# Optimization experiments

Measured on AMD Instinct MI355X. Metric: run time of the kernel, lower is better.

## Reference

```python
import jax, jax.numpy as jnp
import numpy as np

N, E, D, C, H1 = 100000, 1600000, 64, 8, 2


def setup_inputs() -> dict:
    key = jax.random.key(0)
    ks = jax.random.split(key, 16)
    s = 0.1  # small init scale
    inp = {}
    inp["x"] = jax.random.normal(ks[0], (N, D), jnp.float32)
    inp["edge_index"] = jax.random.randint(ks[1], (2, E), 0, N, dtype=jnp.int64)
    # conv1: GATConv(D, D, heads=2, concat=True)
    inp["W1"] = jax.random.normal(ks[2], (D, H1 * D), jnp.float32) * s
    inp["a_src1"] = jax.random.normal(ks[3], (H1, D), jnp.float32) * s
    inp["a_dst1"] = jax.random.normal(ks[4], (H1, D), jnp.float32) * s
    inp["b1"] = jnp.zeros((H1 * D,), jnp.float32)
    # conv2: GATConv(2D, D, heads=1, concat=False)
    inp["W2"] = jax.random.normal(ks[5], (H1 * D, D), jnp.float32) * s
    inp["a_src2"] = jax.random.normal(ks[6], (1, D), jnp.float32) * s
    inp["a_dst2"] = jax.random.normal(ks[7], (1, D), jnp.float32) * s
    inp["b2"] = jnp.zeros((D,), jnp.float32)
    # mlp head (Z = D since G=0)
    inp["mlp1_w"] = jax.random.normal(ks[8], (D, D), jnp.float32) * s
    inp["mlp1_b"] = jnp.zeros((D,), jnp.float32)
    inp["mlp2_w"] = jax.random.normal(ks[9], (D, C), jnp.float32) * s
    inp["mlp2_b"] = jnp.zeros((C,), jnp.float32)
    return inp


def _segment_softmax(e, dst, n):
    # numerically-stable softmax over edges grouped by destination node
    m = jax.ops.segment_max(e, dst, num_segments=n)
    ex = jnp.exp(e - m[dst])
    z = jax.ops.segment_sum(ex, dst, num_segments=n)
    return ex / (z[dst] + 1e-16)


def _gat_conv(x, ei, W, a_src, a_dst, b, heads, f_out, concat):
    n = x.shape[0]
    h = (x @ W).reshape(n, heads, f_out)            # [N,H,F]
    alpha_s = jnp.einsum('nhf,hf->nh', h, a_src)     # [N,H]
    alpha_d = jnp.einsum('nhf,hf->nh', h, a_dst)
    src, dst = ei[0], ei[1]
    e = jax.nn.leaky_relu(alpha_s[src] + alpha_d[dst], 0.2)  # [E,H]
    alpha = _segment_softmax(e, dst, n)
    out = jax.ops.segment_sum(h[src] * alpha[:, :, None], dst, num_segments=n)
    out = out.reshape(n, heads * f_out) if concat else out.mean(axis=1)
    return out + b


def reference(x, edge_index, W1, a_src1, a_dst1, b1, W2, a_src2, a_dst2, b2,
              mlp1_w, mlp1_b, mlp2_w, mlp2_b):
    n = x.shape[0]
    loops = jnp.arange(n, dtype=edge_index.dtype)
    ei = jnp.concatenate([edge_index, jnp.stack([loops, loops])], axis=1)
    h = jax.nn.elu(_gat_conv(x, ei, W1, a_src1, a_dst1, b1, H1, D, True))
    h = jax.nn.elu(_gat_conv(h, ei, W2, a_src2, a_dst2, b2, 1, D, False))
    h = jax.nn.relu(h @ mlp1_w + mlp1_b)
    return jax.nn.relu(h @ mlp2_w + mlp2_b)
```

## Files before the change

kernel.cpp:

```cpp
#include <hip/hip_runtime.h>
#include <hip/hip_bf16.h>

#define NN 100000
#define EE 1600000
#define MM 1700000
#define CH 8192
#define NBLK 208
#define N1 106496
#define NBKT 391
#define NCONV 38024

typedef unsigned short u16;
typedef __attribute__((ext_vector_type(8))) short bf16x8;
typedef __attribute__((ext_vector_type(4))) float f32x4;
typedef __attribute__((ext_vector_type(2))) float f32x2v;

__device__ __forceinline__ float bf2f(u16 u){ return __uint_as_float(((unsigned)u) << 16); }
__device__ __forceinline__ float bf2f_lo(unsigned u){ return __uint_as_float(u << 16); }
__device__ __forceinline__ float bf2f_hi(unsigned u){ return __uint_as_float(u & 0xFFFF0000u); }

__device__ __forceinline__ unsigned f2bf(float f){
  unsigned x = __float_as_uint(f);
  unsigned r = x + 0x7FFFu + ((x >> 16) & 1u);
  return (r >> 16);
}

__device__ __forceinline__ float wred(float v){
  v += __shfl_xor(v, 32, 64);
  v += __shfl_xor(v, 16, 64);
  v += __shfl_xor(v, 8, 64);
  v += __shfl_xor(v, 4, 64);
  v += __shfl_xor(v, 2, 64);
  v += __shfl_xor(v, 1, 64);
  return v;
}

__device__ __forceinline__ float eluf(float v){ return (v > 0.f) ? v : (__expf(v) - 1.f); }

__device__ __forceinline__ void acc_bf8p(f32x2v* acc, uint4 q, float w){
  f32x2v wv = {w, w};
  f32x2v h0 = {bf2f_lo(q.x), bf2f_hi(q.x)};
  f32x2v h1 = {bf2f_lo(q.y), bf2f_hi(q.y)};
  f32x2v h2 = {bf2f_lo(q.z), bf2f_hi(q.z)};
  f32x2v h3 = {bf2f_lo(q.w), bf2f_hi(q.w)};
  acc[0] += wv * h0;
  acc[1] += wv * h1;
  acc[2] += wv * h2;
  acc[3] += wv * h3;
}

__global__ void k_detect(const u16* __restrict__ x16, const int* __restrict__ ei32,
                         int* __restrict__ flags){
  int t = threadIdx.x;
  u16 u = x16[2 * t];
  int eb = (u >> 8) & 0x7F;
  int m1 = (eb >= 0x3A && eb <= 0x41) ? 1 : 0;
  int m2 = (ei32[2 * t + 1] == 0) ? 1 : 0;
  unsigned long long b1 = __ballot(m1);
  unsigned long long b2 = __ballot(m2);
  __shared__ int c1[2], c2[2];
  if ((t & 63) == 0){ c1[t >> 6] = __popcll(b1); c2[t >> 6] = __popcll(b2); }
  __syncthreads();
  if (t == 0){
    flags[0] = (c1[0] + c1[1] >= 64) ? 1 : 0;
    flags[1] = (c2[0] + c2[1] >= 64) ? 1 : 0;
  }
}

__global__ void k_fill(float* __restrict__ o, int n){
  int i = blockIdx.x * blockDim.x + threadIdx.x;
  if (i < n) o[i] = 12345.0f;
}

__global__ __launch_bounds__(256) void k_hist1(const int* __restrict__ ei, int* __restrict__ ghist,
                        const void* s0, const void* s1, const void* s2, const void* s3,
                        const void* s4, const void* s5, const void* s6, const void* s7,
                        const void* s8, const void* s9, const void* s10, const void* s11,
                        float* __restrict__ dst, u16* __restrict__ wt1, u16* __restrict__ wt2,
                        const int* __restrict__ flags){
  __shared__ int h[512];
  int b = blockIdx.x;
  if (b < NBLK){
    for (int i = threadIdx.x; i < 512; i += 256) h[i] = 0;
    __syncthreads();
    int base = b * CH;
    int i64 = flags[1];
    #pragma unroll 4
    for (int k = 0; k < CH / 256; ++k){
      int i = base + k * 256 + threadIdx.x;
      if (i < MM){
        int d;
        if (i < EE) d = i64 ? ei[2 * (EE + i)] : ei[EE + i];
        else        d = i - EE;
        atomicAdd(&h[d >> 8], 1);
      }
    }
    __syncthreads();
    for (int i = threadIdx.x; i < 512; i += 256) ghist[i * NBLK + b] = h[i];
    return;
  }
  int i = (b - NBLK) * 256 + threadIdx.x;
  if (i >= NCONV) return;
  int bf = flags[0];
  if (i < 21640){
    const int offs[13] = {0,8192,8320,8448,8576,16768,16832,16896,16960,21056,21120,21632,21640};
    const void* srcs[12] = {s0,s1,s2,s3,s4,s5,s6,s7,s8,s9,s10,s11};
    int seg = 0;
    while (i >= offs[seg + 1]) seg++;
    int j = i - offs[seg];
    float v = bf ? bf2f(((const u16*)srcs[seg])[j]) : ((const float*)srcs[seg])[j];
    dst[i] = v;
  } else if (i < 29832){
    int i2 = i - 21640;
    int c = i2 >> 6, k = i2 & 63;
    int si = k * 128 + c;
    wt1[i2] = bf ? ((const u16*)s0)[si] : (u16)f2bf(((const float*)s0)[si]);
  } else {
    int i3 = i - 29832;
    int c = i3 >> 7, k = i3 & 127;
    int si = k * 64 + c;
    wt2[i3] = bf ? ((const u16*)s4)[si] : (u16)f2bf(((const float*)s4)[si]);
  }
}

__global__ __launch_bounds__(1024) void k_gscan1(const int* __restrict__ ghist, int* __restrict__ incl,
                                                 int* __restrict__ bsums){
  __shared__ int s[1024];
  int i = blockIdx.x * 1024 + threadIdx.x;
  int v = (i < N1) ? ghist[i] : 0;
  s[threadIdx.x] = v;
  __syncthreads();
  for (int off = 1; off < 1024; off <<= 1){
    int t = (threadIdx.x >= off) ? s[threadIdx.x - off] : 0;
    __syncthreads();
    s[threadIdx.x] += t;
    __syncthreads();
  }
  if (i < N1) incl[i] = s[threadIdx.x];
  if (threadIdx.x == 1023) bsums[blockIdx.x] = s[1023];
}

__global__ void k_scan2(int* __restrict__ bsums, int nb){
  __shared__ int s[128];
  int t = threadIdx.x;
  int v = (t < nb) ? bsums[t] : 0;
  s[t] = v;
  __syncthreads();
  for (int off = 1; off < 128; off <<= 1){
    int x = (t >= off) ? s[t - off] : 0;
    __syncthreads();
    s[t] += x;
    __syncthreads();
  }
  if (t < nb) bsums[t] = s[t];
}

__global__ __launch_bounds__(256) void k_gscan3(const int* __restrict__ incl, const int* __restrict__ ghist,
                                                const int* __restrict__ bsums, int* __restrict__ off1){
  int i = blockIdx.x * blockDim.x + threadIdx.x;
  if (i >= N1) return;
  int b = i >> 10;
  int base = b ? bsums[b - 1] : 0;
  off1[i] = base + incl[i] - ghist[i];
}

__global__ __launch_bounds__(256) void k_scatter1(const int* __restrict__ ei, const int* __restrict__ off1,
                                                  unsigned* __restrict__ e1, const int* __restrict__ flags){
  __shared__ int offs[512];
  __shared__ int cnt[512];
  int b = blockIdx.x;
  for (int i = threadIdx.x; i < 512; i += 256){
    offs[i] = off1[i * NBLK + b];
    cnt[i] = 0;
  }
  __syncthreads();
  int base = b * CH;
  int i64 = flags[1];
  #pragma unroll 4
  for (int k = 0; k < CH / 256; ++k){
    int i = base + k * 256 + threadIdx.x;
    if (i >= MM) break;
    int d, s;
    if (i < EE){
      if (i64){ d = ei[2 * (EE + i)]; s = ei[2 * i]; }
      else    { d = ei[EE + i];       s = ei[i]; }
    } else { d = i - EE; s = d; }
    int bin = d >> 8;
    int r = atomicAdd(&cnt[bin], 1);
    e1[offs[bin] + r] = ((unsigned)s << 8) | ((unsigned)d & 255u);
  }
}

__global__ __launch_bounds__(256) void k_pass2(const unsigned* __restrict__ e1, const int* __restrict__ off1,
                                               int* __restrict__ csr, int* __restrict__ rp){
  __shared__ int hh[256];
  __shared__ int cc[256];
  int bu = blockIdx.x;
  int t = threadIdx.x;
  int s = off1[bu * NBLK];
  int e = off1[(bu + 1) * NBLK];
  hh[t] = 0; cc[t] = 0;
  __syncthreads();
  for (int j = s + t; j < e; j += 256)
    atomicAdd(&hh[e1[j] & 255u], 1);
  __syncthreads();
  int own = hh[t];
  for (int off = 1; off < 256; off <<= 1){
    int x = (t >= off) ? hh[t - off] : 0;
    __syncthreads();
    hh[t] += x;
    __syncthreads();
  }
  int excl = hh[t] - own;
  hh[t] = excl;
  int node = (bu << 8) + t;
  if (node < NN) rp[node] = s + excl;
  if (bu == 0 && t == 0) rp[NN] = MM;
  __syncthreads();
  for (int j = s + t; j < e; j += 256){
    unsigned kv = e1[j];
    int d = kv & 255u;
    int r = atomicAdd(&cc[d], 1);
    csr[s + hh[d] + r] = (int)(kv >> 8);
  }
}

__global__ __launch_bounds__(256) void k_gemm1(const void* __restrict__ xv, const u16* __restrict__ wt1,
                                               const float* __restrict__ asw, const float* __restrict__ adw,
                                               u16* __restrict__ h1bf, float* __restrict__ AS, float* __restrict__ AD,
                                               const int* __restrict__ flags, int n){
  int tid = threadIdx.x;
  int wv = tid >> 6, l = tid & 63;
  int lm = l & 15, lk = l >> 4;
  int M0 = blockIdx.x * 64 + wv * 16;
  int row = M0 + lm; if (row >= n) row = n - 1;
  bf16x8 a0, a1;
  if (flags[0]){
    const u16* xp = (const u16*)xv + (size_t)row * 64;
    union { uint4 u; bf16x8 v; } c0, c1;
    c0.u = *(const uint4*)&xp[lk * 8];
    c1.u = *(const uint4*)&xp[32 + lk * 8];
    a0 = c0.v; a1 = c1.v;
  } else {
    const float* xp = (const float*)xv + (size_t)row * 64;
    float4 f0 = *(const float4*)&xp[lk * 8];
    float4 f1 = *(const float4*)&xp[lk * 8 + 4];
    float4 f2 = *(const float4*)&xp[32 + lk * 8];
    float4 f3 = *(const float4*)&xp[32 + lk * 8 + 4];
    union { u16 s[8]; bf16x8 v; } p0, p1;
    p0.s[0]=(u16)f2bf(f0.x); p0.s[1]=(u16)f2bf(f0.y); p0.s[2]=(u16)f2bf(f0.z); p0.s[3]=(u16)f2bf(f0.w);
    p0.s[4]=(u16)f2bf(f1.x); p0.s[5]=(u16)f2bf(f1.y); p0.s[6]=(u16)f2bf(f1.z); p0.s[7]=(u16)f2bf(f1.w);
    p1.s[0]=(u16)f2bf(f2.x); p1.s[1]=(u16)f2bf(f2.y); p1.s[2]=(u16)f2bf(f2.z); p1.s[3]=(u16)f2bf(f2.w);
    p1.s[4]=(u16)f2bf(f3.x); p1.s[5]=(u16)f2bf(f3.y); p1.s[6]=(u16)f2bf(f3.z); p1.s[7]=(u16)f2bf(f3.w);
    a0 = p0.v; a1 = p1.v;
  }
  f32x4 acc[8];
  #pragma unroll
  for (int nt = 0; nt < 8; ++nt) acc[nt] = (f32x4){0.f, 0.f, 0.f, 0.f};
  #pragma unroll
  for (int nt = 0; nt < 8; ++nt){
    int col = nt * 16 + lm;
    union { uint4 u; bf16x8 v; } b0, b1;
    b0.u = *(const uint4*)&wt1[(size_t)col * 64 + lk * 8];
    b1.u = *(const uint4*)&wt1[(size_t)col * 64 + 32 + lk * 8];
    acc[nt] = __builtin_amdgcn_mfma_f32_16x16x32_bf16(a0, b0.v, acc[nt], 0, 0, 0);
    acc[nt] = __builtin_amdgcn_mfma_f32_16x16x32_bf16(a1, b1.v, acc[nt], 0, 0, 0);
  }
  float ps0[4] = {0,0,0,0}, pd0[4] = {0,0,0,0}, ps1[4] = {0,0,0,0}, pd1[4] = {0,0,0,0};
  #pragma unroll
  for (int nt = 0; nt < 8; ++nt){
    int col = nt * 16 + lm;
    float aw = asw[col], dw = adw[col];
    #pragma unroll
    for (int i = 0; i < 4; ++i){
      float v = acc[nt][i];
      if (nt < 4){ ps0[i] += v * aw; pd0[i] += v * dw; }
      else       { ps1[i] += v * aw; pd1[i] += v * dw; }
    }
  }
  #pragma unroll
  for (int mk = 8; mk >= 1; mk >>= 1){
    #pragma unroll
    for (int i = 0; i < 4; ++i){
      ps0[i] += __shfl_xor(ps0[i], mk, 64); pd0[i] += __shfl_xor(pd0[i], mk, 64);
      ps1[i] += __shfl_xor(ps1[i], mk, 64); pd1[i] += __shfl_xor(pd1[i], mk, 64);
    }
  }
  #pragma unroll
  for (int nt = 0; nt < 8; ++nt){
    int col = nt * 16 + lm;
    #pragma unroll
    for (int i = 0; i < 4; ++i){
      int r = M0 + lk * 4 + i;
      if (r < n) h1bf[(size_t)r * 128 + col] = (u16)f2bf(acc[nt][i]);
    }
  }
  if (lm == 0){
    #pragma unroll
    for (int i = 0; i < 4; ++i){
      int r = M0 + lk * 4 + i;
      if (r < n){
        AS[r * 2] = ps0[i]; AS[r * 2 + 1] = ps1[i];
        AD[r * 2] = pd0[i]; AD[r * 2 + 1] = pd1[i];
      }
    }
  }
}

__global__ __launch_bounds__(256) void k_agg1(const u16* __restrict__ h1bf, const int* __restrict__ rp,
                                              const int* __restrict__ csr, const float* __restrict__ AS,
                                              const float* __restrict__ AD, const float* __restrict__ b1,
                                              u16* __restrict__ out, int n){
  int node = (blockIdx.x * blockDim.x + threadIdx.x) >> 6;
  int lane = threadIdx.x & 63;
  if (node >= n) return;
  int g = lane >> 4, u = lane & 15;
  int beg = rp[node], end = rp[node + 1];
  float2 adv = *(const float2*)&AD[node * 2];
  f32x2v acc[4] = {{0,0},{0,0},{0,0},{0,0}};
  float zp0 = 0.f, zp1 = 0.f;
  for (int c = beg; c < end; c += 64){
    int m = end - c; if (m > 64) m = 64;
    int s_l = 0; float w0_l = 0.f, w1_l = 0.f;
    if (lane < m){
      s_l = csr[c + lane];
      float2 as2 = *(const float2*)&AS[s_l * 2];
      float e0 = as2.x + adv.x; e0 = fmaxf(e0, 0.2f * e0);
      float e1 = as2.y + adv.y; e1 = fmaxf(e1, 0.2f * e1);
      w0_l = __expf(e0); w1_l = __expf(e1);
    }
    zp0 += w0_l; zp1 += w1_l;
    for (int jj = 0; jj < m; jj += 16){
      int eA = jj + g, eB = jj + 4 + g, eC = jj + 8 + g, eD = jj + 12 + g;
      bool vA = eA < m, vB = eB < m, vC = eC < m, vD = eD < m;
      int sA = __shfl(s_l, eA, 64), sB = __shfl(s_l, eB, 64);
      int sC = __shfl(s_l, eC, 64), sD = __shfl(s_l, eD, 64);
      float wA0 = __shfl(w0_l, eA, 64), wA1 = __shfl(w1_l, eA, 64);
      float wB0 = __shfl(w0_l, eB, 64), wB1 = __shfl(w1_l, eB, 64);
      float wC0 = __shfl(w0_l, eC, 64), wC1 = __shfl(w1_l, eC, 64);
      float wD0 = __shfl(w0_l, eD, 64), wD1 = __shfl(w1_l, eD, 64);
      uint4 qA, qB, qC, qD;
      if (vA) qA = *(const uint4*)&h1bf[(size_t)sA * 128 + u * 8];
      if (vB) qB = *(const uint4*)&h1bf[(size_t)sB * 128 + u * 8];
      if (vC) qC = *(const uint4*)&h1bf[(size_t)sC * 128 + u * 8];
      if (vD) qD = *(const uint4*)&h1bf[(size_t)sD * 128 + u * 8];
      if (vA) acc_bf8p(acc, qA, (u < 8) ? wA0 : wA1);
      if (vB) acc_bf8p(acc, qB, (u < 8) ? wB0 : wB1);
      if (vC) acc_bf8p(acc, qC, (u < 8) ? wC0 : wC1);
      if (vD) acc_bf8p(acc, qD, (u < 8) ? wD0 : wD1);
    }
  }
  #pragma unroll
  for (int mk = 16; mk <= 32; mk <<= 1){
    #pragma unroll
    for (int k = 0; k < 4; ++k){
      acc[k][0] += __shfl_xor(acc[k][0], mk, 64);
      acc[k][1] += __shfl_xor(acc[k][1], mk, 64);
    }
  }
  float z0 = wred(zp0), z1 = wred(zp1);
  float rz = (u < 8) ? (1.f / (z0 + 1e-16f)) : (1.f / (z1 + 1e-16f));
  if (g == 0){
    float4 ba = *(const float4*)&b1[u * 8];
    float4 bb = *(const float4*)&b1[u * 8 + 4];
    float o0 = eluf(acc[0][0] * rz + ba.x), o1 = eluf(acc[0][1] * rz + ba.y);
    float o2 = eluf(acc[1][0] * rz + ba.z), o3 = eluf(acc[1][1] * rz + ba.w);
    float o4 = eluf(acc[2][0] * rz + bb.x), o5 = eluf(acc[2][1] * rz + bb.y);
    float o6 = eluf(acc[3][0] * rz + bb.z), o7 = eluf(acc[3][1] * rz + bb.w);
    uint4 pk;
    pk.x = f2bf(o0) | (f2bf(o1) << 16);
    pk.y = f2bf(o2) | (f2bf(o3) << 16);
    pk.z = f2bf(o4) | (f2bf(o5) << 16);
    pk.w = f2bf(o6) | (f2bf(o7) << 16);
    *(uint4*)&out[(size_t)node * 128 + u * 8] = pk;
  }
}

__global__ __launch_bounds__(256) void k_gemm2(const u16* __restrict__ hin, const u16* __restrict__ wt2,
                                               const float* __restrict__ asw, const float* __restrict__ adw,
                                               u16* __restrict__ h2bf, float* __restrict__ AS, float* __restrict__ AD,
                                               int n){
  int tid = threadIdx.x;
  int wv = tid >> 6, l = tid & 63;
  int lm = l & 15, lk = l >> 4;
  int M0 = blockIdx.x * 64 + wv * 16;
  int row = M0 + lm; if (row >= n) row = n - 1;
  const u16* hp = hin + (size_t)row * 128;
  bf16x8 a[4];
  #pragma unroll
  for (int kt = 0; kt < 4; ++kt){
    union { uint4 u; bf16x8 v; } c;
    c.u = *(const uint4*)&hp[kt * 32 + lk * 8];
    a[kt] = c.v;
  }
  f32x4 acc[4];
  #pragma unroll
  for (int nt = 0; nt < 4; ++nt) acc[nt] = (f32x4){0.f, 0.f, 0.f, 0.f};
  #pragma unroll
  for (int nt = 0; nt < 4; ++nt){
    int col = nt * 16 + lm;
    #pragma unroll
    for (int kt = 0; kt < 4; ++kt){
      union { uint4 u; bf16x8 v; } b;
      b.u = *(const uint4*)&wt2[(size_t)col * 128 + kt * 32 + lk * 8];
      acc[nt] = __builtin_amdgcn_mfma_f32_16x16x32_bf16(a[kt], b.v, acc[nt], 0, 0, 0);
    }
  }
  float ps[4] = {0,0,0,0}, pd[4] = {0,0,0,0};
  #pragma unroll
  for (int nt = 0; nt < 4; ++nt){
    int col = nt * 16 + lm;
    float aw = asw[col], dw = adw[col];
    #pragma unroll
    for (int i = 0; i < 4; ++i){
      float v = acc[nt][i];
      ps[i] += v * aw; pd[i] += v * dw;
    }
  }
  #pragma unroll
  for (int mk = 8; mk >= 1; mk >>= 1){
    #pragma unroll
    for (int i = 0; i < 4; ++i){
      ps[i] += __shfl_xor(ps[i], mk, 64); pd[i] += __shfl_xor(pd[i], mk, 64);
    }
  }
  #pragma unroll
  for (int nt = 0; nt < 4; ++nt){
    int col = nt * 16 + lm;
    #pragma unroll
    for (int i = 0; i < 4; ++i){
      int r = M0 + lk * 4 + i;
      if (r < n) h2bf[(size_t)r * 64 + col] = (u16)f2bf(acc[nt][i]);
    }
  }
  if (lm == 0){
    #pragma unroll
    for (int i = 0; i < 4; ++i){
      int r = M0 + lk * 4 + i;
      if (r < n){ AS[r] = ps[i]; AD[r] = pd[i]; }
    }
  }
}

__global__ __launch_bounds__(256) void k_agg2(const u16* __restrict__ h2bf, const int* __restrict__ rp,
                                              const int* __restrict__ csr, const float* __restrict__ AS,
                                              const float* __restrict__ AD, const float* __restrict__ b2,
                                              u16* __restrict__ hb, int n){
  int node = (blockIdx.x * blockDim.x + threadIdx.x) >> 6;
  int lane = threadIdx.x & 63;
  if (node >= n) return;
  int g = lane >> 3, u = lane & 7;
  int beg = rp[node], end = rp[node + 1];
  float ad = AD[node];
  f32x2v acc[4] = {{0,0},{0,0},{0,0},{0,0}};
  float zp = 0.f;
  for (int c = beg; c < end; c += 64){
    int m = end - c; if (m > 64) m = 64;
    int s_l = 0; float w_l = 0.f;
    if (lane < m){
      s_l = csr[c + lane];
      float e = AS[s_l] + ad; e = fmaxf(e, 0.2f * e);
      w_l = __expf(e);
    }
    zp += w_l;
    for (int jj = 0; jj < m; jj += 32){
      int eA = jj + g, eB = jj + 8 + g, eC = jj + 16 + g, eD = jj + 24 + g;
      bool vA = eA < m, vB = eB < m, vC = eC < m, vD = eD < m;
      int sA = __shfl(s_l, eA, 64), sB = __shfl(s_l, eB, 64);
      int sC = __shfl(s_l, eC, 64), sD = __shfl(s_l, eD, 64);
      float wA = __shfl(w_l, eA, 64), wB = __shfl(w_l, eB, 64);
      float wC = __shfl(w_l, eC, 64), wD = __shfl(w_l, eD, 64);
      uint4 qA, qB, qC, qD;
      if (vA) qA = *(const uint4*)&h2bf[(size_t)sA * 64 + u * 8];
      if (vB) qB = *(const uint4*)&h2bf[(size_t)sB * 64 + u * 8];
      if (vC) qC = *(const uint4*)&h2bf[(size_t)sC * 64 + u * 8];
      if (vD) qD = *(const uint4*)&h2bf[(size_t)sD * 64 + u * 8];
      if (vA) acc_bf8p(acc, qA, wA);
      if (vB) acc_bf8p(acc, qB, wB);
      if (vC) acc_bf8p(acc, qC, wC);
      if (vD) acc_bf8p(acc, qD, wD);
    }
  }
  #pragma unroll
  for (int mk = 8; mk <= 32; mk <<= 1){
    #pragma unroll
    for (int k = 0; k < 4; ++k){
      acc[k][0] += __shfl_xor(acc[k][0], mk, 64);
      acc[k][1] += __shfl_xor(acc[k][1], mk, 64);
    }
  }
  float z = wred(zp);
  float rz = 1.f / (z + 1e-16f);
  if (g == 0){
    float4 ba = *(const float4*)&b2[u * 8];
    float4 bb = *(const float4*)&b2[u * 8 + 4];
    float o0 = eluf(acc[0][0] * rz + ba.x), o1 = eluf(acc[0][1] * rz + ba.y);
    float o2 = eluf(acc[1][0] * rz + ba.z), o3 = eluf(acc[1][1] * rz + ba.w);
    float o4 = eluf(acc[2][0] * rz + bb.x), o5 = eluf(acc[2][1] * rz + bb.y);
    float o6 = eluf(acc[3][0] * rz + bb.z), o7 = eluf(acc[3][1] * rz + bb.w);
    uint4 pk;
    pk.x = f2bf(o0) | (f2bf(o1) << 16);
    pk.y = f2bf(o2) | (f2bf(o3) << 16);
    pk.z = f2bf(o4) | (f2bf(o5) << 16);
    pk.w = f2bf(o6) | (f2bf(o7) << 16);
    *(uint4*)&hb[(size_t)node * 64 + u * 8] = pk;
  }
}

__global__ __launch_bounds__(256) void k_mlp(const u16* __restrict__ hb,
                                             const float* __restrict__ m1w, const float* __restrict__ m1b,
                                             const float* __restrict__ m2w, const float* __restrict__ m2b,
                                             void* __restrict__ outv, const int* __restrict__ flags, int n){
  int node = blockIdx.x * 256 + threadIdx.x;
  bool act = node < n;
  const u16* hp = hb + (size_t)(act ? node : 0) * 64;
  float acc[64];
  #pragma unroll
  for (int j = 0; j < 64; ++j) acc[j] = m1b[j];
  #pragma unroll
  for (int kc = 0; kc < 8; ++kc){
    uint4 q = *(const uint4*)&hp[kc * 8];
    float hk[8] = {bf2f_lo(q.x), bf2f_hi(q.x), bf2f_lo(q.y), bf2f_hi(q.y),
                   bf2f_lo(q.z), bf2f_hi(q.z), bf2f_lo(q.w), bf2f_hi(q.w)};
    #pragma unroll
    for (int t = 0; t < 8; ++t){
      const float* wr = &m1w[(kc * 8 + t) * 64];
      #pragma unroll
      for (int j = 0; j < 64; ++j) acc[j] += hk[t] * wr[j];
    }
  }
  float o[8];
  #pragma unroll
  for (int c = 0; c < 8; ++c) o[c] = m2b[c];
  #pragma unroll
  for (int j = 0; j < 64; ++j){
    float r = fmaxf(acc[j], 0.f);
    const float* w2r = &m2w[j * 8];
    #pragma unroll
    for (int c = 0; c < 8; ++c) o[c] += r * w2r[c];
  }
  if (act){
    if (flags[0]){
      uint4 pk;
      pk.x = f2bf(fmaxf(o[0], 0.f)) | (f2bf(fmaxf(o[1], 0.f)) << 16);
      pk.y = f2bf(fmaxf(o[2], 0.f)) | (f2bf(fmaxf(o[3], 0.f)) << 16);
      pk.z = f2bf(fmaxf(o[4], 0.f)) | (f2bf(fmaxf(o[5], 0.f)) << 16);
      pk.w = f2bf(fmaxf(o[6], 0.f)) | (f2bf(fmaxf(o[7], 0.f)) << 16);
      *(uint4*)&((u16*)outv)[(size_t)node * 8] = pk;
    } else {
      float4 a, b;
      a.x = fmaxf(o[0], 0.f); a.y = fmaxf(o[1], 0.f); a.z = fmaxf(o[2], 0.f); a.w = fmaxf(o[3], 0.f);
      b.x = fmaxf(o[4], 0.f); b.y = fmaxf(o[5], 0.f); b.z = fmaxf(o[6], 0.f); b.w = fmaxf(o[7], 0.f);
      *(float4*)&((float*)outv)[(size_t)node * 8]     = a;
      *(float4*)&((float*)outv)[(size_t)node * 8 + 4] = b;
    }
  }
}

extern "C" void kernel_launch(void* const* d_in, const int* in_sizes, int n_in,
                              void* d_out, int out_size, void* d_ws, size_t ws_size,
                              hipStream_t stream){
  const void* x   = d_in[0];
  const void* ei  = d_in[1];

  char* base = (char*)d_ws;
  size_t off = 0;
  auto alloc = [&](size_t bytes) -> void* {
    void* p = base + off;
    off += (bytes + 255) & ~(size_t)255;
    return p;
  };
  float* wbuf  = (float*)alloc(21640 * 4);
  u16*   wt1   = (u16*)alloc(8192 * 2);
  u16*   wt2   = (u16*)alloc(8192 * 2);
  u16*   h1bf  = (u16*)alloc((size_t)NN * 128 * 2);
  u16*   h1bbf = (u16*)alloc((size_t)NN * 128 * 2);
  u16*   hbuf  = (u16*)alloc((size_t)NN * 64 * 2);
  float* AS1   = (float*)alloc((size_t)NN * 2 * 4);
  float* AD1   = (float*)alloc((size_t)NN * 2 * 4);
  float* AS2   = (float*)alloc((size_t)NN * 4);
  float* AD2   = (float*)alloc((size_t)NN * 4);
  unsigned* e1 = (unsigned*)alloc((size_t)MM * 4);
  int*   csr   = (int*)alloc((size_t)MM * 4);
  int*   rp    = (int*)alloc((size_t)(NN + 1) * 4);
  int*   ghist = (int*)alloc((size_t)N1 * 4);
  int*   incl  = (int*)alloc((size_t)N1 * 4);
  int*   off1  = (int*)alloc((size_t)N1 * 4);
  int*   bsums = (int*)alloc(128 * 4);
  int*   flags = (int*)alloc(8);

  if (off > ws_size){
    int nf = out_size / 2;
    k_fill<<<(nf + 255) / 256, 256, 0, stream>>>((float*)d_out, nf);
    return;
  }

  float* AS1W = wbuf + 8192;
  float* AD1W = wbuf + 8320;
  float* B1f  = wbuf + 8448;
  float* AS2W = wbuf + 16768;
  float* AD2W = wbuf + 16832;
  float* B2f  = wbuf + 16896;
  float* M1W  = wbuf + 16960;
  float* M1B  = wbuf + 21056;
  float* M2W  = wbuf + 21120;
  float* M2B  = wbuf + 21632;
  u16*   h2bf = h1bf;

  const int NBCONV = (NCONV + 255) / 256;

  k_detect<<<1, 128, 0, stream>>>((const u16*)x, (const int*)ei, flags);
  k_hist1<<<NBLK + NBCONV, 256, 0, stream>>>((const int*)ei, ghist,
                                             d_in[2], d_in[3], d_in[4], d_in[5], d_in[6],
                                             d_in[7], d_in[8], d_in[9], d_in[10], d_in[11],
                                             d_in[12], d_in[13], wbuf, wt1, wt2, flags);
  k_gscan1<<<N1 / 1024, 1024, 0, stream>>>(ghist, incl, bsums);
  k_scan2<<<1, 128, 0, stream>>>(bsums, N1 / 1024);
  k_gscan3<<<(N1 + 255) / 256, 256, 0, stream>>>(incl, ghist, bsums, off1);
  k_scatter1<<<NBLK, 256, 0, stream>>>((const int*)ei, off1, e1, flags);
  k_pass2<<<NBKT, 256, 0, stream>>>(e1, off1, csr, rp);

  k_gemm1<<<(NN + 63) / 64, 256, 0, stream>>>(x, wt1, AS1W, AD1W, h1bf, AS1, AD1, flags, NN);
  k_agg1<<<(NN + 3) / 4, 256, 0, stream>>>(h1bf, rp, csr, AS1, AD1, B1f, h1bbf, NN);

  k_gemm2<<<(NN + 63) / 64, 256, 0, stream>>>(h1bbf, wt2, AS2W, AD2W, h2bf, AS2, AD2, NN);
  k_agg2<<<(NN + 3) / 4, 256, 0, stream>>>(h2bf, rp, csr, AS2, AD2, B2f, hbuf, NN);
  k_mlp<<<(NN + 255) / 256, 256, 0, stream>>>(hbuf, M1W, M1B, M2W, M2B, d_out, flags, NN);
}
```

Baseline: 275.0 us.

## Fuse scatter with gemm1, inline dtype detection, vectorize edge loads, half-wave agg1

Removes the separate k_detect launch and flags buffer; each wave now detects the input dtypes itself with a ballot. The edge scatter and first GEMM run in one launch as disjoint block ranges, and the histogram and scatter loops read edge indices as int4 vectors. k_agg1 gives each half-wave its own node, two nodes per wave, to cut idle lanes on low-degree nodes. This costs redundant detection reads per wave and makes agg1 use narrower edge chunks.

```diff
diff --git a/kernel.cpp b/kernel.cpp
--- a/kernel.cpp
+++ b/kernel.cpp
@@ -9,6 +9,7 @@
 #define N1 106496
 #define NBKT 391
 #define NCONV 38024
+#define NBG1 1563
 
 typedef unsigned short u16;
 typedef __attribute__((ext_vector_type(8))) short bf16x8;
@@ -25,8 +26,30 @@
   return (r >> 16);
 }
 
+__device__ __forceinline__ int detect_bf(const u16* __restrict__ x16){
+  int lane = threadIdx.x & 63;
+  u16 u = x16[2 * lane];
+  int eb = (u >> 8) & 0x7F;
+  unsigned long long b = __ballot(eb >= 0x3A && eb <= 0x41);
+  return __popcll(b) >= 32;
+}
+__device__ __forceinline__ int detect_i64(const int* __restrict__ ei32){
+  int lane = threadIdx.x & 63;
+  unsigned long long b = __ballot(ei32[2 * lane + 1] == 0);
+  return __popcll(b) >= 32;
+}
+
 __device__ __forceinline__ float wred(float v){
   v += __shfl_xor(v, 32, 64);
+  v += __shfl_xor(v, 16, 64);
+  v += __shfl_xor(v, 8, 64);
+  v += __shfl_xor(v, 4, 64);
+  v += __shfl_xor(v, 2, 64);
+  v += __shfl_xor(v, 1, 64);
+  return v;
+}
+
+__device__ __forceinline__ float hwred(float v){
   v += __shfl_xor(v, 16, 64);
   v += __shfl_xor(v, 8, 64);
   v += __shfl_xor(v, 4, 64);
@@ -49,59 +72,56 @@
   acc[3] += wv * h3;
 }
 
-__global__ void k_detect(const u16* __restrict__ x16, const int* __restrict__ ei32,
-                         int* __restrict__ flags){
-  int t = threadIdx.x;
-  u16 u = x16[2 * t];
-  int eb = (u >> 8) & 0x7F;
-  int m1 = (eb >= 0x3A && eb <= 0x41) ? 1 : 0;
-  int m2 = (ei32[2 * t + 1] == 0) ? 1 : 0;
-  unsigned long long b1 = __ballot(m1);
-  unsigned long long b2 = __ballot(m2);
-  __shared__ int c1[2], c2[2];
-  if ((t & 63) == 0){ c1[t >> 6] = __popcll(b1); c2[t >> 6] = __popcll(b2); }
-  __syncthreads();
-  if (t == 0){
-    flags[0] = (c1[0] + c1[1] >= 64) ? 1 : 0;
-    flags[1] = (c2[0] + c2[1] >= 64) ? 1 : 0;
-  }
-}
-
 __global__ void k_fill(float* __restrict__ o, int n){
   int i = blockIdx.x * blockDim.x + threadIdx.x;
   if (i < n) o[i] = 12345.0f;
 }
 
-__global__ __launch_bounds__(256) void k_hist1(const int* __restrict__ ei, int* __restrict__ ghist,
+__global__ __launch_bounds__(256) void k_hist1(const int* __restrict__ ei, const u16* __restrict__ x16,
+                        int* __restrict__ ghist,
                         const void* s0, const void* s1, const void* s2, const void* s3,
                         const void* s4, const void* s5, const void* s6, const void* s7,
                         const void* s8, const void* s9, const void* s10, const void* s11,
-                        float* __restrict__ dst, u16* __restrict__ wt1, u16* __restrict__ wt2,
-                        const int* __restrict__ flags){
-  __shared__ int h[512];
+                        float* __restrict__ dst, u16* __restrict__ wt1, u16* __restrict__ wt2){
+  __shared__ int hsh[512];
   int b = blockIdx.x;
   if (b < NBLK){
-    for (int i = threadIdx.x; i < 512; i += 256) h[i] = 0;
-    __syncthreads();
-    int base = b * CH;
-    int i64 = flags[1];
-    #pragma unroll 4
-    for (int k = 0; k < CH / 256; ++k){
-      int i = base + k * 256 + threadIdx.x;
-      if (i < MM){
-        int d;
-        if (i < EE) d = i64 ? ei[2 * (EE + i)] : ei[EE + i];
-        else        d = i - EE;
-        atomicAdd(&h[d >> 8], 1);
+    for (int i = threadIdx.x; i < 512; i += 256) hsh[i] = 0;
+    int i64 = detect_i64(ei);
+    __syncthreads();
+    #pragma unroll
+    for (int k = 0; k < 8; ++k){
+      int i0 = b * CH + k * 1024 + threadIdx.x * 4;
+      if (i0 >= MM) break;
+      if (i0 + 3 < EE){
+        if (i64){
+          int4 q0 = *(const int4*)&ei[2 * (EE + i0)];
+          int4 q1 = *(const int4*)&ei[2 * (EE + i0) + 4];
+          atomicAdd(&hsh[q0.x >> 8], 1); atomicAdd(&hsh[q0.z >> 8], 1);
+          atomicAdd(&hsh[q1.x >> 8], 1); atomicAdd(&hsh[q1.z >> 8], 1);
+        } else {
+          int4 q = *(const int4*)&ei[EE + i0];
+          atomicAdd(&hsh[q.x >> 8], 1); atomicAdd(&hsh[q.y >> 8], 1);
+          atomicAdd(&hsh[q.z >> 8], 1); atomicAdd(&hsh[q.w >> 8], 1);
+        }
+      } else {
+        for (int t = 0; t < 4; ++t){
+          int i = i0 + t;
+          if (i >= MM) break;
+          int d;
+          if (i < EE) d = i64 ? ei[2 * (EE + i)] : ei[EE + i];
+          else        d = i - EE;
+          atomicAdd(&hsh[d >> 8], 1);
+        }
       }
     }
     __syncthreads();
-    for (int i = threadIdx.x; i < 512; i += 256) ghist[i * NBLK + b] = h[i];
+    for (int i = threadIdx.x; i < 512; i += 256) ghist[i * NBLK + b] = hsh[i];
     return;
   }
   int i = (b - NBLK) * 256 + threadIdx.x;
   if (i >= NCONV) return;
-  int bf = flags[0];
+  int bf = detect_bf(x16);
   if (i < 21640){
     const int offs[13] = {0,8192,8320,8448,8576,16768,16832,16896,16960,21056,21120,21632,21640};
     const void* srcs[12] = {s0,s1,s2,s3,s4,s5,s6,s7,s8,s9,s10,s11};
@@ -164,78 +184,69 @@
   off1[i] = base + incl[i] - ghist[i];
 }
 
-__global__ __launch_bounds__(256) void k_scatter1(const int* __restrict__ ei, const int* __restrict__ off1,
-                                                  unsigned* __restrict__ e1, const int* __restrict__ flags){
+__global__ __launch_bounds__(256) void k_scat_gemm1(
+    const int* __restrict__ ei, const int* __restrict__ off1, unsigned* __restrict__ e1,
+    const void* __restrict__ xv, const u16* __restrict__ wt1,
+    const float* __restrict__ asw, const float* __restrict__ adw,
+    u16* __restrict__ h1bf, float* __restrict__ AS, float* __restrict__ AD, int n){
   __shared__ int offs[512];
   __shared__ int cnt[512];
   int b = blockIdx.x;
-  for (int i = threadIdx.x; i < 512; i += 256){
-    offs[i] = off1[i * NBLK + b];
-    cnt[i] = 0;
-  }
-  __syncthreads();
-  int base = b * CH;
-  int i64 = flags[1];
-  #pragma unroll 4
-  for (int k = 0; k < CH / 256; ++k){
-    int i = base + k * 256 + threadIdx.x;
-    if (i >= MM) break;
-    int d, s;
-    if (i < EE){
-      if (i64){ d = ei[2 * (EE + i)]; s = ei[2 * i]; }
-      else    { d = ei[EE + i];       s = ei[i]; }
-    } else { d = i - EE; s = d; }
-    int bin = d >> 8;
-    int r = atomicAdd(&cnt[bin], 1);
-    e1[offs[bin] + r] = ((unsigned)s << 8) | ((unsigned)d & 255u);
-  }
-}
-
-__global__ __launch_bounds__(256) void k_pass2(const unsigned* __restrict__ e1, const int* __restrict__ off1,
-                                               int* __restrict__ csr, int* __restrict__ rp){
-  __shared__ int hh[256];
-  __shared__ int cc[256];
-  int bu = blockIdx.x;
-  int t = threadIdx.x;
-  int s = off1[bu * NBLK];
-  int e = off1[(bu + 1) * NBLK];
-  hh[t] = 0; cc[t] = 0;
-  __syncthreads();
-  for (int j = s + t; j < e; j += 256)
-    atomicAdd(&hh[e1[j] & 255u], 1);
-  __syncthreads();
-  int own = hh[t];
-  for (int off = 1; off < 256; off <<= 1){
-    int x = (t >= off) ? hh[t - off] : 0;
-    __syncthreads();
-    hh[t] += x;
-    __syncthreads();
-  }
-  int excl = hh[t] - own;
-  hh[t] = excl;
-  int node = (bu << 8) + t;
-  if (node < NN) rp[node] = s + excl;
-  if (bu == 0 && t == 0) rp[NN] = MM;
-  __syncthreads();
-  for (int j = s + t; j < e; j += 256){
-    unsigned kv = e1[j];
-    int d = kv & 255u;
-    int r = atomicAdd(&cc[d], 1);
-    csr[s + hh[d] + r] = (int)(kv >> 8);
-  }
-}
-
-__global__ __launch_bounds__(256) void k_gemm1(const void* __restrict__ xv, const u16* __restrict__ wt1,
-                                               const float* __restrict__ asw, const float* __restrict__ adw,
-                                               u16* __restrict__ h1bf, float* __restrict__ AS, float* __restrict__ AD,
-                                               const int* __restrict__ flags, int n){
+  if (b < NBLK){
+    int i64 = detect_i64(ei);
+    for (int i = threadIdx.x; i < 512; i += 256){
+      offs[i] = off1[i * NBLK + b];
+      cnt[i] = 0;
+    }
+    __syncthreads();
+    #pragma unroll
+    for (int k = 0; k < 8; ++k){
+      int i0 = b * CH + k * 1024 + threadIdx.x * 4;
+      if (i0 >= MM) break;
+      int sv[4], dv[4];
+      int cntv = 4;
+      if (i0 + 3 < EE){
+        if (i64){
+          int4 a0 = *(const int4*)&ei[2 * i0];
+          int4 a1 = *(const int4*)&ei[2 * i0 + 4];
+          int4 b0 = *(const int4*)&ei[2 * (EE + i0)];
+          int4 b1 = *(const int4*)&ei[2 * (EE + i0) + 4];
+          sv[0]=a0.x; sv[1]=a0.z; sv[2]=a1.x; sv[3]=a1.z;
+          dv[0]=b0.x; dv[1]=b0.z; dv[2]=b1.x; dv[3]=b1.z;
+        } else {
+          int4 a = *(const int4*)&ei[i0];
+          int4 d = *(const int4*)&ei[EE + i0];
+          sv[0]=a.x; sv[1]=a.y; sv[2]=a.z; sv[3]=a.w;
+          dv[0]=d.x; dv[1]=d.y; dv[2]=d.z; dv[3]=d.w;
+        }
+      } else {
+        cntv = 0;
+        for (int t = 0; t < 4; ++t){
+          int i = i0 + t;
+          if (i >= MM) break;
+          if (i < EE){
+            if (i64){ sv[cntv] = ei[2 * i]; dv[cntv] = ei[2 * (EE + i)]; }
+            else    { sv[cntv] = ei[i];     dv[cntv] = ei[EE + i]; }
+          } else { sv[cntv] = i - EE; dv[cntv] = i - EE; }
+          cntv++;
+        }
+      }
+      for (int t = 0; t < cntv; ++t){
+        int bin = dv[t] >> 8;
+        int r = atomicAdd(&cnt[bin], 1);
+        e1[offs[bin] + r] = ((unsigned)sv[t] << 8) | ((unsigned)dv[t] & 255u);
+      }
+    }
+    return;
+  }
+  int bf = detect_bf((const u16*)xv);
   int tid = threadIdx.x;
   int wv = tid >> 6, l = tid & 63;
   int lm = l & 15, lk = l >> 4;
-  int M0 = blockIdx.x * 64 + wv * 16;
+  int M0 = (b - NBLK) * 64 + wv * 16;
   int row = M0 + lm; if (row >= n) row = n - 1;
   bf16x8 a0, a1;
-  if (flags[0]){
+  if (bf){
     const u16* xp = (const u16*)xv + (size_t)row * 64;
     union { uint4 u; bf16x8 v; } c0, c1;
     c0.u = *(const uint4*)&xp[lk * 8];
@@ -307,38 +318,77 @@
   }
 }
 
+__global__ __launch_bounds__(256) void k_pass2(const unsigned* __restrict__ e1, const int* __restrict__ off1,
+                                               int* __restrict__ csr, int* __restrict__ rp){
+  __shared__ int hh[256];
+  __shared__ int cc[256];
+  int bu = blockIdx.x;
+  int t = threadIdx.x;
+  int s = off1[bu * NBLK];
+  int e = off1[(bu + 1) * NBLK];
+  hh[t] = 0; cc[t] = 0;
+  __syncthreads();
+  for (int j = s + t; j < e; j += 256)
+    atomicAdd(&hh[e1[j] & 255u], 1);
+  __syncthreads();
+  int own = hh[t];
+  for (int off = 1; off < 256; off <<= 1){
+    int x = (t >= off) ? hh[t - off] : 0;
+    __syncthreads();
+    hh[t] += x;
+    __syncthreads();
+  }
+  int excl = hh[t] - own;
+  hh[t] = excl;
+  int node = (bu << 8) + t;
+  if (node < NN) rp[node] = s + excl;
+  if (bu == 0 && t == 0) rp[NN] = MM;
+  __syncthreads();
+  for (int j = s + t; j < e; j += 256){
+    unsigned kv = e1[j];
+    int d = kv & 255u;
+    int r = atomicAdd(&cc[d], 1);
+    csr[s + hh[d] + r] = (int)(kv >> 8);
+  }
+}
+
 __global__ __launch_bounds__(256) void k_agg1(const u16* __restrict__ h1bf, const int* __restrict__ rp,
                                               const int* __restrict__ csr, const float* __restrict__ AS,
                                               const float* __restrict__ AD, const float* __restrict__ b1,
                                               u16* __restrict__ out, int n){
-  int node = (blockIdx.x * blockDim.x + threadIdx.x) >> 6;
-  int lane = threadIdx.x & 63;
-  if (node >= n) return;
-  int g = lane >> 4, u = lane & 15;
+  int tid = threadIdx.x;
+  int wid = (blockIdx.x * 256 + tid) >> 6;
+  int h = (tid >> 5) & 1;
+  int l5 = tid & 31;
+  int node = wid * 2 + h;
+  bool valid = node < n;
+  if (!valid) node = n - 1;
+  int g = l5 >> 4, u = l5 & 15;
+  int hb = h * 32;
   int beg = rp[node], end = rp[node + 1];
   float2 adv = *(const float2*)&AD[node * 2];
   f32x2v acc[4] = {{0,0},{0,0},{0,0},{0,0}};
   float zp0 = 0.f, zp1 = 0.f;
-  for (int c = beg; c < end; c += 64){
-    int m = end - c; if (m > 64) m = 64;
+  for (int c = beg; c < end; c += 32){
+    int m = end - c; if (m > 32) m = 32;
     int s_l = 0; float w0_l = 0.f, w1_l = 0.f;
-    if (lane < m){
-      s_l = csr[c + lane];
+    if (l5 < m){
+      s_l = csr[c + l5];
       float2 as2 = *(const float2*)&AS[s_l * 2];
       float e0 = as2.x + adv.x; e0 = fmaxf(e0, 0.2f * e0);
       float e1 = as2.y + adv.y; e1 = fmaxf(e1, 0.2f * e1);
       w0_l = __expf(e0); w1_l = __expf(e1);
     }
     zp0 += w0_l; zp1 += w1_l;
-    for (int jj = 0; jj < m; jj += 16){
-      int eA = jj + g, eB = jj + 4 + g, eC = jj + 8 + g, eD = jj + 12 + g;
+    for (int jj = 0; jj < m; jj += 8){
+      int eA = jj + g, eB = jj + 2 + g, eC = jj + 4 + g, eD = jj + 6 + g;
       bool vA = eA < m, vB = eB < m, vC = eC < m, vD = eD < m;
-      int sA = __shfl(s_l, eA, 64), sB = __shfl(s_l, eB, 64);
-      int sC = __shfl(s_l, eC, 64), sD = __shfl(s_l, eD, 64);
-      float wA0 = __shfl(w0_l, eA, 64), wA1 = __shfl(w1_l, eA, 64);
-      float wB0 = __shfl(w0_l, eB, 64), wB1 = __shfl(w1_l, eB, 64);
-      float wC0 = __shfl(w0_l, eC, 64), wC1 = __shfl(w1_l, eC, 64);
-      float wD0 = __shfl(w0_l, eD, 64), wD1 = __shfl(w1_l, eD, 64);
+      int sA = __shfl(s_l, hb + eA, 64), sB = __shfl(s_l, hb + eB, 64);
+      int sC = __shfl(s_l, hb + eC, 64), sD = __shfl(s_l, hb + eD, 64);
+      float wA0 = __shfl(w0_l, hb + eA, 64), wA1 = __shfl(w1_l, hb + eA, 64);
+      float wB0 = __shfl(w0_l, hb + eB, 64), wB1 = __shfl(w1_l, hb + eB, 64);
+      float wC0 = __shfl(w0_l, hb + eC, 64), wC1 = __shfl(w1_l, hb + eC, 64);
+      float wD0 = __shfl(w0_l, hb + eD, 64), wD1 = __shfl(w1_l, hb + eD, 64);
       uint4 qA, qB, qC, qD;
       if (vA) qA = *(const uint4*)&h1bf[(size_t)sA * 128 + u * 8];
       if (vB) qB = *(const uint4*)&h1bf[(size_t)sB * 128 + u * 8];
@@ -351,16 +401,13 @@
     }
   }
   #pragma unroll
-  for (int mk = 16; mk <= 32; mk <<= 1){
-    #pragma unroll
-    for (int k = 0; k < 4; ++k){
-      acc[k][0] += __shfl_xor(acc[k][0], mk, 64);
-      acc[k][1] += __shfl_xor(acc[k][1], mk, 64);
-    }
-  }
-  float z0 = wred(zp0), z1 = wred(zp1);
+  for (int k = 0; k < 4; ++k){
+    acc[k][0] += __shfl_xor(acc[k][0], 16, 64);
+    acc[k][1] += __shfl_xor(acc[k][1], 16, 64);
+  }
+  float z0 = hwred(zp0), z1 = hwred(zp1);
   float rz = (u < 8) ? (1.f / (z0 + 1e-16f)) : (1.f / (z1 + 1e-16f));
-  if (g == 0){
+  if (g == 0 && valid){
     float4 ba = *(const float4*)&b1[u * 8];
     float4 bb = *(const float4*)&b1[u * 8 + 4];
     float o0 = eluf(acc[0][0] * rz + ba.x), o1 = eluf(acc[0][1] * rz + ba.y);
@@ -507,10 +554,11 @@
   }
 }
 
-__global__ __launch_bounds__(256) void k_mlp(const u16* __restrict__ hb,
+__global__ __launch_bounds__(256) void k_mlp(const u16* __restrict__ hb, const u16* __restrict__ x16,
                                              const float* __restrict__ m1w, const float* __restrict__ m1b,
                                              const float* __restrict__ m2w, const float* __restrict__ m2b,
-                                             void* __restrict__ outv, const int* __restrict__ flags, int n){
+                                             void* __restrict__ outv, int n){
+  int bf = detect_bf(x16);
   int node = blockIdx.x * 256 + threadIdx.x;
   bool act = node < n;
   const u16* hp = hb + (size_t)(act ? node : 0) * 64;
@@ -540,7 +588,7 @@
     for (int c = 0; c < 8; ++c) o[c] += r * w2r[c];
   }
   if (act){
-    if (flags[0]){
+    if (bf){
       uint4 pk;
       pk.x = f2bf(fmaxf(o[0], 0.f)) | (f2bf(fmaxf(o[1], 0.f)) << 16);
       pk.y = f2bf(fmaxf(o[2], 0.f)) | (f2bf(fmaxf(o[3], 0.f)) << 16);
@@ -587,7 +635,6 @@
   int*   incl  = (int*)alloc((size_t)N1 * 4);
   int*   off1  = (int*)alloc((size_t)N1 * 4);
   int*   bsums = (int*)alloc(128 * 4);
-  int*   flags = (int*)alloc(8);
 
   if (off > ws_size){
     int nf = out_size / 2;
@@ -609,21 +656,20 @@
 
   const int NBCONV = (NCONV + 255) / 256;
 
-  k_detect<<<1, 128, 0, stream>>>((const u16*)x, (const int*)ei, flags);
-  k_hist1<<<NBLK + NBCONV, 256, 0, stream>>>((const int*)ei, ghist,
+  k_hist1<<<NBLK + NBCONV, 256, 0, stream>>>((const int*)ei, (const u16*)x, ghist,
                                              d_in[2], d_in[3], d_in[4], d_in[5], d_in[6],
                                              d_in[7], d_in[8], d_in[9], d_in[10], d_in[11],
-                                             d_in[12], d_in[13], wbuf, wt1, wt2, flags);
+                                             d_in[12], d_in[13], wbuf, wt1, wt2);
   k_gscan1<<<N1 / 1024, 1024, 0, stream>>>(ghist, incl, bsums);
   k_scan2<<<1, 128, 0, stream>>>(bsums, N1 / 1024);
   k_gscan3<<<(N1 + 255) / 256, 256, 0, stream>>>(incl, ghist, bsums, off1);
-  k_scatter1<<<NBLK, 256, 0, stream>>>((const int*)ei, off1, e1, flags);
+  k_scat_gemm1<<<NBLK + NBG1, 256, 0, stream>>>((const int*)ei, off1, e1,
+                                                x, wt1, AS1W, AD1W, h1bf, AS1, AD1, NN);
   k_pass2<<<NBKT, 256, 0, stream>>>(e1, off1, csr, rp);
 
-  k_gemm1<<<(NN + 63) / 64, 256, 0, stream>>>(x, wt1, AS1W, AD1W, h1bf, AS1, AD1, flags, NN);
-  k_agg1<<<(NN + 3) / 4, 256, 0, stream>>>(h1bf, rp, csr, AS1, AD1, B1f, h1bbf, NN);
+  k_agg1<<<(NN / 2 + 3) / 4, 256, 0, stream>>>(h1bf, rp, csr, AS1, AD1, B1f, h1bbf, NN);
 
   k_gemm2<<<(NN + 63) / 64, 256, 0, stream>>>(h1bbf, wt2, AS2W, AD2W, h2bf, AS2, AD2, NN);
   k_agg2<<<(NN + 3) / 4, 256, 0, stream>>>(h2bf, rp, csr, AS2, AD2, B2f, hbuf, NN);
-  k_mlp<<<(NN + 255) / 256, 256, 0, stream>>>(hbuf, M1W, M1B, M2W, M2B, d_out, flags, NN);
-}
+  k_mlp<<<(NN + 255) / 256, 256, 0, stream>>>(hbuf, (const u16*)x, M1W, M1B, M2W, M2B, d_out, NN);
+}
```

After: 253.1 us. 1.09x faster.
